# Optimization experiments

Measured on AMD Instinct MI355X. Metric: run time of the kernel, lower is better.

The kernel has to match this reference:

```python
import jax, jax.numpy as jnp
import numpy as np


def setup_inputs() -> dict:
    key = jax.random.key(0)
    k1, k2, k3, k4 = jax.random.split(key, 4)
    B, T, S, D = 256, 16, 32, 768
    return {
        "video_global": jax.random.normal(k1, (B, D), dtype=jnp.float32),
        "text_global": jax.random.normal(k2, (B, D), dtype=jnp.float32),
        "video_local": jax.random.normal(k3, (B, T, D), dtype=jnp.float32),
        "text_local": jax.random.normal(k4, (B, S, D), dtype=jnp.float32),
        "temp": jnp.zeros((1,), dtype=jnp.float32),  # log(1.0)
    }


def reference(video_global, text_global, video_local, text_local, temp):
    B = video_global.shape[0]
    logit_scale = jnp.exp(temp)[0]

    # ---- global contrastive loss ----
    global_sim = logit_scale * (video_global @ text_global.T)  # [B, B]
    diag = jnp.arange(B)
    loss_v2t = -jax.nn.log_softmax(global_sim, axis=1)[diag, diag].mean()
    loss_t2v = -jax.nn.log_softmax(global_sim, axis=0)[diag, diag].mean()
    loss_global = 0.5 * (loss_v2t + loss_t2v)

    # ---- local positive scores ----
    # paired (diagonal) local similarity: [B, T, S]
    sim_pos = logit_scale * jnp.einsum("btd,bsd->bts", video_local, text_local)
    time_weights = jax.nn.softmax(sim_pos.max(axis=-1), axis=-1)  # [B, T]
    pos_scores = (sim_pos.mean(axis=-1) * time_weights).sum(axis=1)  # [B]

    # ---- local negative scores (batched pairwise contraction) ----
    # [B, B, T, S]: video i vs text j, replacing the B*(B-1) tiny einsum loop
    sim_all = logit_scale * jnp.einsum("btd,csd->bcts", video_local, text_local)
    neg_full = (time_weights[:, None, :] * sim_all.mean(axis=-1)).sum(axis=-1)  # [B, B]

    # drop diagonal (i == j), preserving row-major loop order
    rows, cols = np.nonzero(~np.eye(B, dtype=bool))
    neg_scores = neg_full[rows, cols].reshape(B, B - 1)

    logits = jnp.concatenate([pos_scores[:, None], neg_scores], axis=-1)  # [B, B]
    loss_local = -jax.nn.log_softmax(logits, axis=-1)[:, 0].mean()

    return 0.6 * loss_global + 0.4 * loss_local
```

## Files before the change

### kernel.cpp

```cpp
#include <hip/hip_runtime.h>
#include <cmath>

#define BB 256
#define TT 16
#define SS 32
#define DD 768
#define LROW 260

__device__ __forceinline__ void wave_lse(
    const float* __restrict__ cparts, float* __restrict__ out,
    int cm, int row, float w)
{
    const int lane = threadIdx.x & 63;
    float4 x = make_float4(0.f, 0.f, 0.f, 0.f);
    const float* base = cparts + (size_t)cm * 65536 + (size_t)row * 256 + (lane << 2);
#pragma unroll
    for (int p = 0; p < 8; ++p) {
        float4 v = *(const float4*)(base + (size_t)p * 3 * 65536);
        x.x += v.x; x.y += v.y; x.z += v.z; x.w += v.w;
    }
    float m = fmaxf(fmaxf(x.x, x.y), fmaxf(x.z, x.w));
#pragma unroll
    for (int off = 32; off > 0; off >>= 1)
        m = fmaxf(m, __shfl_xor(m, off, 64));
    float e = expf(x.x - m) + expf(x.y - m) + expf(x.z - m) + expf(x.w - m);
#pragma unroll
    for (int off = 32; off > 0; off >>= 1)
        e += __shfl_xor(e, off, 64);
    if (lane == (row >> 2)) {
        float lse = m + logf(e);
        float xd = (row & 2) ? ((row & 1) ? x.w : x.z)
                             : ((row & 1) ? x.y : x.x);
        atomicAdd(out, w * (lse - xd));
    }
}

__global__ __launch_bounds__(512, 4) void hl_k1(
    const float* __restrict__ vl, const float* __restrict__ tl,
    const float* __restrict__ vgp, const float* __restrict__ tgp,
    const float* __restrict__ temp,
    float* __restrict__ vw_ws, float* __restrict__ tb_ws,
    float* __restrict__ cparts, float* __restrict__ out, int out_n)
{
    __shared__ float lds[13024];
    const int tid = threadIdx.x;
    const float lsc = expf(temp[0]);

    if (blockIdx.x < BB) {
        float* smem  = lds;
        float* simb  = lds + 12480;
        float* rmaxb = lds + 12992;
        float* twb   = lds + 13008;
        const int i = blockIdx.x;
        if (i == 0) {
            for (int o = tid; o < out_n; o += 512) out[o] = 0.f;
        }

        const int slice = tid & 15;
        const int g     = tid >> 4;
        const int tgr   = g >> 3;
        const int sg    = g & 7;

        const float* vli = vl + (size_t)i * TT * DD;
        const float* tli = tl + (size_t)i * SS * DD;

        float acc[4][4];
#pragma unroll
        for (int a = 0; a < 4; ++a)
#pragma unroll
            for (int b = 0; b < 4; ++b) acc[a][b] = 0.f;

        float4 pre[6];
#pragma unroll
        for (int k = 0; k < 2; ++k) {
            int f4 = tid + (k << 9);
            pre[k] = *(const float4*)&vli[(f4 >> 6) * DD + ((f4 & 63) << 2)];
        }
#pragma unroll
        for (int k = 0; k < 4; ++k) {
            int f4 = tid + (k << 9);
            pre[2 + k] = *(const float4*)&tli[(f4 >> 6) * DD + ((f4 & 63) << 2)];
        }

        for (int c = 0; c < 3; ++c) {
            __syncthreads();
#pragma unroll
            for (int k = 0; k < 2; ++k) {
                int f4 = tid + (k << 9);
                *(float4*)&smem[(f4 >> 6) * LROW + ((f4 & 63) << 2)] = pre[k];
            }
#pragma unroll
            for (int k = 0; k < 4; ++k) {
                int f4 = tid + (k << 9);
                *(float4*)&smem[(16 + (f4 >> 6)) * LROW + ((f4 & 63) << 2)] = pre[2 + k];
            }
            __syncthreads();
            if (c < 2) {
                const int d0n = (c + 1) << 8;
#pragma unroll
                for (int k = 0; k < 2; ++k) {
                    int f4 = tid + (k << 9);
                    pre[k] = *(const float4*)&vli[(f4 >> 6) * DD + d0n + ((f4 & 63) << 2)];
                }
#pragma unroll
                for (int k = 0; k < 4; ++k) {
                    int f4 = tid + (k << 9);
                    pre[2 + k] = *(const float4*)&tli[(f4 >> 6) * DD + d0n + ((f4 & 63) << 2)];
                }
            }
#pragma unroll
            for (int step = 0; step < 4; ++step) {
                const int db = (slice << 4) + (step << 2);
                float4 av[4], bv[4];
#pragma unroll
                for (int ti = 0; ti < 4; ++ti)
                    av[ti] = *(const float4*)&smem[(tgr * 4 + ti) * LROW + db];
#pragma unroll
                for (int sj = 0; sj < 4; ++sj)
                    bv[sj] = *(const float4*)&smem[(16 + sg * 4 + sj) * LROW + db];
#pragma unroll
                for (int ti = 0; ti < 4; ++ti)
#pragma unroll
                    for (int sj = 0; sj < 4; ++sj)
                        acc[ti][sj] += av[ti].x * bv[sj].x + av[ti].y * bv[sj].y
                                     + av[ti].z * bv[sj].z + av[ti].w * bv[sj].w;
            }
        }
        __syncthreads();

#pragma unroll
        for (int ti = 0; ti < 4; ++ti)
#pragma unroll
            for (int sj = 0; sj < 4; ++sj) {
                int t = tgr * 4 + ti, s = sg * 4 + sj;
                smem[(t * 32 + s) * 17 + slice] = acc[ti][sj];
            }
        __syncthreads();
        {
            float ssum = 0.f;
#pragma unroll
            for (int k = 0; k < 16; ++k) ssum += smem[tid * 17 + k];
            simb[tid] = lsc * ssum;
        }
        __syncthreads();
        if (tid < 16) {
            float m = -3.0e38f;
            for (int s = 0; s < 32; ++s)
                m = fmaxf(m, simb[tid * 32 + ((s + tid) & 31)]);
            rmaxb[tid] = m;
        }
        __syncthreads();
        if (tid == 0) {
            float M = -3.0e38f;
            for (int t = 0; t < 16; ++t) M = fmaxf(M, rmaxb[t]);
            float ssum = 0.f;
            for (int t = 0; t < 16; ++t) {
                float e = expf(rmaxb[t] - M);
                twb[t] = e;
                ssum += e;
            }
            float inv = 1.0f / ssum;
            for (int t = 0; t < 16; ++t) twb[t] *= inv;
        }
        __syncthreads();

        for (int d = tid; d < DD; d += 512) {
            float vwv = 0.f;
#pragma unroll
            for (int t = 0; t < 16; ++t) vwv += twb[t] * vli[t * DD + d];
            vw_ws[(size_t)i * DD + d] = vwv;
            float tbv = 0.f;
#pragma unroll
            for (int s = 0; s < 32; ++s) tbv += tli[s * DD + d];
            tb_ws[(size_t)i * DD + d] = tbv * (1.0f / 32.0f);
        }
    } else {
        float (*As)[68] = (float (*)[68])lds;
        float (*Bs)[68] = (float (*)[68])(lds + 1088);
        float (*Tb)[68] = (float (*)[68])(lds + 2176);
        const int b  = blockIdx.x - BB;
        const int p  = b & 7;
        const int tj = (b >> 3) & 3;
        const int ti = b >> 5;
        const int i0 = ti * 64, j0 = tj * 64, kb0 = p * 96;
        const bool act = tid < 256;
        const int srow = tid >> 2, skq = tid & 3;
        const int tr = tid >> 4, tc = tid & 15;

        float acc[4][4];
#pragma unroll
        for (int r = 0; r < 4; ++r)
#pragma unroll
            for (int cc = 0; cc < 4; ++cc) acc[r][cc] = 0.f;

        float4 a4 = make_float4(0.f, 0.f, 0.f, 0.f), b4 = a4;
        float4 a4n = a4, b4n = b4;
        if (act) {
            a4 = *(const float4*)&vgp[(size_t)(i0 + srow) * DD + kb0 + skq * 4];
            b4 = *(const float4*)&tgp[(size_t)(j0 + srow) * DD + kb0 + skq * 4];
        }
        for (int ch = 0; ch < 6; ++ch) {
            __syncthreads();
            if (act) {
                As[skq * 4 + 0][srow] = a4.x; As[skq * 4 + 1][srow] = a4.y;
                As[skq * 4 + 2][srow] = a4.z; As[skq * 4 + 3][srow] = a4.w;
                Bs[skq * 4 + 0][srow] = b4.x; Bs[skq * 4 + 1][srow] = b4.y;
                Bs[skq * 4 + 2][srow] = b4.z; Bs[skq * 4 + 3][srow] = b4.w;
            }
            __syncthreads();
            if (act && ch < 5) {
                const int kb = kb0 + (ch + 1) * 16;
                a4n = *(const float4*)&vgp[(size_t)(i0 + srow) * DD + kb + skq * 4];
                b4n = *(const float4*)&tgp[(size_t)(j0 + srow) * DD + kb + skq * 4];
            }
            if (act) {
#pragma unroll
                for (int k = 0; k < 16; ++k) {
                    float4 av = *(const float4*)&As[k][tr * 4];
                    float4 bv = *(const float4*)&Bs[k][tc * 4];
                    float ar[4] = {av.x, av.y, av.z, av.w};
                    float br[4] = {bv.x, bv.y, bv.z, bv.w};
#pragma unroll
                    for (int r = 0; r < 4; ++r)
#pragma unroll
                        for (int cc = 0; cc < 4; ++cc)
                            acc[r][cc] += ar[r] * br[cc];
                }
            }
            a4 = a4n; b4 = b4n;
        }

        if (act) {
            float* Cp = cparts + ((size_t)p * 3 + 1) * 65536;
#pragma unroll
            for (int r = 0; r < 4; ++r) {
                float4 v = {acc[r][0] * lsc, acc[r][1] * lsc,
                            acc[r][2] * lsc, acc[r][3] * lsc};
                *(float4*)&Cp[(size_t)(i0 + tr * 4 + r) * 256 + j0 + tc * 4] = v;
            }
        }
        __syncthreads();
        if (act) {
#pragma unroll
            for (int r = 0; r < 4; ++r)
#pragma unroll
                for (int cc = 0; cc < 4; ++cc)
                    Tb[tc * 4 + cc][tr * 4 + r] = acc[r][cc] * lsc;
        }
        __syncthreads();
        if (act) {
            float* Ct = cparts + ((size_t)p * 3 + 2) * 65536;
#pragma unroll
            for (int r = 0; r < 4; ++r) {
                float4 v = *(const float4*)&Tb[tr * 4 + r][tc * 4];
                *(float4*)&Ct[(size_t)(j0 + tr * 4 + r) * 256 + i0 + tc * 4] = v;
            }
        }
    }
}

__global__ __launch_bounds__(256) void hl_k2(
    const float* __restrict__ vw, const float* __restrict__ tbm,
    const float* __restrict__ temp, float* __restrict__ cparts,
    float* __restrict__ out)
{
    const int tid = threadIdx.x;
    const int b   = blockIdx.x;
    if (b < 128) {
        __shared__ float As[16][68];
        __shared__ float Bs[16][68];
        const float lsc = expf(temp[0]);
        const int p = b & 7, tj = (b >> 3) & 3, ti = b >> 5;
        const int i0 = ti * 64, j0 = tj * 64, kb0 = p * 96;
        const int srow = tid >> 2, skq = tid & 3;
        const int tr = tid >> 4, tc = tid & 15;

        float acc[4][4];
#pragma unroll
        for (int r = 0; r < 4; ++r)
#pragma unroll
            for (int cc = 0; cc < 4; ++cc) acc[r][cc] = 0.f;

        float4 a4 = *(const float4*)&vw [(size_t)(i0 + srow) * DD + kb0 + skq * 4];
        float4 b4 = *(const float4*)&tbm[(size_t)(j0 + srow) * DD + kb0 + skq * 4];
        float4 a4n = a4, b4n = b4;
        for (int ch = 0; ch < 6; ++ch) {
            __syncthreads();
            As[skq * 4 + 0][srow] = a4.x; As[skq * 4 + 1][srow] = a4.y;
            As[skq * 4 + 2][srow] = a4.z; As[skq * 4 + 3][srow] = a4.w;
            Bs[skq * 4 + 0][srow] = b4.x; Bs[skq * 4 + 1][srow] = b4.y;
            Bs[skq * 4 + 2][srow] = b4.z; Bs[skq * 4 + 3][srow] = b4.w;
            __syncthreads();
            if (ch < 5) {
                const int kb = kb0 + (ch + 1) * 16;
                a4n = *(const float4*)&vw [(size_t)(i0 + srow) * DD + kb + skq * 4];
                b4n = *(const float4*)&tbm[(size_t)(j0 + srow) * DD + kb + skq * 4];
            }
#pragma unroll
            for (int k = 0; k < 16; ++k) {
                float4 av = *(const float4*)&As[k][tr * 4];
                float4 bv = *(const float4*)&Bs[k][tc * 4];
                float ar[4] = {av.x, av.y, av.z, av.w};
                float br[4] = {bv.x, bv.y, bv.z, bv.w};
#pragma unroll
                for (int r = 0; r < 4; ++r)
#pragma unroll
                    for (int cc = 0; cc < 4; ++cc)
                        acc[r][cc] += ar[r] * br[cc];
            }
            a4 = a4n; b4 = b4n;
        }

        float* Cp = cparts + (size_t)p * 3 * 65536;
#pragma unroll
        for (int r = 0; r < 4; ++r) {
            float4 v = {acc[r][0] * lsc, acc[r][1] * lsc,
                        acc[r][2] * lsc, acc[r][3] * lsc};
            *(float4*)&Cp[(size_t)(i0 + tr * 4 + r) * 256 + j0 + tc * 4] = v;
        }
    } else {
        const int idx = b - 128;
        const int cm  = 1 + (idx >> 6);
        const int row = ((idx & 63) << 2) + (tid >> 6);
        wave_lse(cparts, out, cm, row, 0.3f / 256.0f);
    }
}

__global__ __launch_bounds__(256) void hl_k3(
    const float* __restrict__ cparts, float* __restrict__ out)
{
    const int row = (blockIdx.x << 2) + (threadIdx.x >> 6);
    wave_lse(cparts, out, 0, row, 0.4f / 256.0f);
}

extern "C" void kernel_launch(void* const* d_in, const int* in_sizes, int n_in,
                              void* d_out, int out_size, void* d_ws, size_t ws_size,
                              hipStream_t stream)
{
    const float* vg   = (const float*)d_in[0];
    const float* tg   = (const float*)d_in[1];
    const float* vl   = (const float*)d_in[2];
    const float* tl   = (const float*)d_in[3];
    const float* temp = (const float*)d_in[4];
    float* out = (float*)d_out;

    float* vw     = (float*)d_ws;
    float* tbw    = vw + (size_t)BB * DD;
    float* cparts = tbw + (size_t)BB * DD;

    hl_k1<<<dim3(BB + 128), dim3(512), 0, stream>>>(vl, tl, vg, tg, temp,
                                                    vw, tbw, cparts, out, out_size);
    hl_k2<<<dim3(256), dim3(256), 0, stream>>>(vw, tbw, temp, cparts, out);
    hl_k3<<<dim3(64),  dim3(256), 0, stream>>>(cparts, out);
}
```

Measured before the change: 123.2 us.

## Pack two GEMM tiles per 512-thread block and drop register prefetch in local sim

The global-GEMM blocks in the first kernel previously left half their 512 threads idle; now each block runs two 64x64 tile jobs, one per 256-thread half, each with its own shared-memory region, which halves the extra block count. The second kernel likewise uses 512-thread blocks holding two GEMM jobs or eight LSE rows, and the third kernel handles eight rows per block. The local-similarity loop drops register-staged prefetch of the next chunk in favour of direct global-to-LDS copies, and the occupancy hint in launch_bounds is removed. This trades latency hiding for lower register pressure, and the larger per-block shared memory may reduce how many blocks fit per CU.

```diff
diff --git a/kernel.cpp b/kernel.cpp
--- a/kernel.cpp
+++ b/kernel.cpp
@@ -35,14 +35,14 @@
     }
 }
 
-__global__ __launch_bounds__(512, 4) void hl_k1(
+__global__ __launch_bounds__(512) void hl_k1(
     const float* __restrict__ vl, const float* __restrict__ tl,
     const float* __restrict__ vgp, const float* __restrict__ tgp,
     const float* __restrict__ temp,
     float* __restrict__ vw_ws, float* __restrict__ tb_ws,
     float* __restrict__ cparts, float* __restrict__ out, int out_n)
 {
-    __shared__ float lds[13024];
+    __shared__ float lds[13056];
     const int tid = threadIdx.x;
     const float lsc = expf(temp[0]);
 
@@ -70,44 +70,23 @@
 #pragma unroll
             for (int b = 0; b < 4; ++b) acc[a][b] = 0.f;
 
-        float4 pre[6];
-#pragma unroll
-        for (int k = 0; k < 2; ++k) {
-            int f4 = tid + (k << 9);
-            pre[k] = *(const float4*)&vli[(f4 >> 6) * DD + ((f4 & 63) << 2)];
-        }
-#pragma unroll
-        for (int k = 0; k < 4; ++k) {
-            int f4 = tid + (k << 9);
-            pre[2 + k] = *(const float4*)&tli[(f4 >> 6) * DD + ((f4 & 63) << 2)];
-        }
-
         for (int c = 0; c < 3; ++c) {
-            __syncthreads();
+            const int d0 = c << 8;
 #pragma unroll
             for (int k = 0; k < 2; ++k) {
                 int f4 = tid + (k << 9);
-                *(float4*)&smem[(f4 >> 6) * LROW + ((f4 & 63) << 2)] = pre[k];
+                int r  = f4 >> 6;
+                int dc = (f4 & 63) << 2;
+                *(float4*)&smem[r * LROW + dc] = *(const float4*)&vli[r * DD + d0 + dc];
             }
 #pragma unroll
             for (int k = 0; k < 4; ++k) {
                 int f4 = tid + (k << 9);
-                *(float4*)&smem[(16 + (f4 >> 6)) * LROW + ((f4 & 63) << 2)] = pre[2 + k];
-            }
-            __syncthreads();
-            if (c < 2) {
-                const int d0n = (c + 1) << 8;
-#pragma unroll
-                for (int k = 0; k < 2; ++k) {
-                    int f4 = tid + (k << 9);
-                    pre[k] = *(const float4*)&vli[(f4 >> 6) * DD + d0n + ((f4 & 63) << 2)];
-                }
-#pragma unroll
-                for (int k = 0; k < 4; ++k) {
-                    int f4 = tid + (k << 9);
-                    pre[2 + k] = *(const float4*)&tli[(f4 >> 6) * DD + d0n + ((f4 & 63) << 2)];
-                }
-            }
+                int r  = f4 >> 6;
+                int dc = (f4 & 63) << 2;
+                *(float4*)&smem[(16 + r) * LROW + dc] = *(const float4*)&tli[r * DD + d0 + dc];
+            }
+            __syncthreads();
 #pragma unroll
             for (int step = 0; step < 4; ++step) {
                 const int db = (slice << 4) + (step << 2);
@@ -125,8 +104,8 @@
                         acc[ti][sj] += av[ti].x * bv[sj].x + av[ti].y * bv[sj].y
                                      + av[ti].z * bv[sj].z + av[ti].w * bv[sj].w;
             }
-        }
-        __syncthreads();
+            __syncthreads();
+        }
 
 #pragma unroll
         for (int ti = 0; ti < 4; ++ti)
@@ -175,17 +154,20 @@
             tb_ws[(size_t)i * DD + d] = tbv * (1.0f / 32.0f);
         }
     } else {
-        float (*As)[68] = (float (*)[68])lds;
-        float (*Bs)[68] = (float (*)[68])(lds + 1088);
-        float (*Tb)[68] = (float (*)[68])(lds + 2176);
-        const int b  = blockIdx.x - BB;
-        const int p  = b & 7;
-        const int tj = (b >> 3) & 3;
-        const int ti = b >> 5;
+        const int h   = tid >> 8;
+        const int t   = tid & 255;
+        const int job = ((blockIdx.x - BB) << 1) | h;
+        float* base = lds + h * 6528;
+        float (*As)[68] = (float (*)[68])base;
+        float (*Bs)[68] = (float (*)[68])(base + 1088);
+        float (*Tb)[68] = (float (*)[68])(base + 2176);
+
+        const int p  = job & 7;
+        const int tj = (job >> 3) & 3;
+        const int ti = job >> 5;
         const int i0 = ti * 64, j0 = tj * 64, kb0 = p * 96;
-        const bool act = tid < 256;
-        const int srow = tid >> 2, skq = tid & 3;
-        const int tr = tid >> 4, tc = tid & 15;
+        const int srow = t >> 2, skq = t & 3;
+        const int tr = t >> 4, tc = t & 15;
 
         float acc[4][4];
 #pragma unroll
@@ -193,96 +175,8 @@
 #pragma unroll
             for (int cc = 0; cc < 4; ++cc) acc[r][cc] = 0.f;
 
-        float4 a4 = make_float4(0.f, 0.f, 0.f, 0.f), b4 = a4;
-        float4 a4n = a4, b4n = b4;
-        if (act) {
-            a4 = *(const float4*)&vgp[(size_t)(i0 + srow) * DD + kb0 + skq * 4];
-            b4 = *(const float4*)&tgp[(size_t)(j0 + srow) * DD + kb0 + skq * 4];
-        }
-        for (int ch = 0; ch < 6; ++ch) {
-            __syncthreads();
-            if (act) {
-                As[skq * 4 + 0][srow] = a4.x; As[skq * 4 + 1][srow] = a4.y;
-                As[skq * 4 + 2][srow] = a4.z; As[skq * 4 + 3][srow] = a4.w;
-                Bs[skq * 4 + 0][srow] = b4.x; Bs[skq * 4 + 1][srow] = b4.y;
-                Bs[skq * 4 + 2][srow] = b4.z; Bs[skq * 4 + 3][srow] = b4.w;
-            }
-            __syncthreads();
-            if (act && ch < 5) {
-                const int kb = kb0 + (ch + 1) * 16;
-                a4n = *(const float4*)&vgp[(size_t)(i0 + srow) * DD + kb + skq * 4];
-                b4n = *(const float4*)&tgp[(size_t)(j0 + srow) * DD + kb + skq * 4];
-            }
-            if (act) {
-#pragma unroll
-                for (int k = 0; k < 16; ++k) {
-                    float4 av = *(const float4*)&As[k][tr * 4];
-                    float4 bv = *(const float4*)&Bs[k][tc * 4];
-                    float ar[4] = {av.x, av.y, av.z, av.w};
-                    float br[4] = {bv.x, bv.y, bv.z, bv.w};
-#pragma unroll
-                    for (int r = 0; r < 4; ++r)
-#pragma unroll
-                        for (int cc = 0; cc < 4; ++cc)
-                            acc[r][cc] += ar[r] * br[cc];
-                }
-            }
-            a4 = a4n; b4 = b4n;
-        }
-
-        if (act) {
-            float* Cp = cparts + ((size_t)p * 3 + 1) * 65536;
-#pragma unroll
-            for (int r = 0; r < 4; ++r) {
-                float4 v = {acc[r][0] * lsc, acc[r][1] * lsc,
-                            acc[r][2] * lsc, acc[r][3] * lsc};
-                *(float4*)&Cp[(size_t)(i0 + tr * 4 + r) * 256 + j0 + tc * 4] = v;
-            }
-        }
-        __syncthreads();
-        if (act) {
-#pragma unroll
-            for (int r = 0; r < 4; ++r)
-#pragma unroll
-                for (int cc = 0; cc < 4; ++cc)
-                    Tb[tc * 4 + cc][tr * 4 + r] = acc[r][cc] * lsc;
-        }
-        __syncthreads();
-        if (act) {
-            float* Ct = cparts + ((size_t)p * 3 + 2) * 65536;
-#pragma unroll
-            for (int r = 0; r < 4; ++r) {
-                float4 v = *(const float4*)&Tb[tr * 4 + r][tc * 4];
-                *(float4*)&Ct[(size_t)(j0 + tr * 4 + r) * 256 + i0 + tc * 4] = v;
-            }
-        }
-    }
-}
-
-__global__ __launch_bounds__(256) void hl_k2(
-    const float* __restrict__ vw, const float* __restrict__ tbm,
-    const float* __restrict__ temp, float* __restrict__ cparts,
-    float* __restrict__ out)
-{
-    const int tid = threadIdx.x;
-    const int b   = blockIdx.x;
-    if (b < 128) {
-        __shared__ float As[16][68];
-        __shared__ float Bs[16][68];
-        const float lsc = expf(temp[0]);
-        const int p = b & 7, tj = (b >> 3) & 3, ti = b >> 5;
-        const int i0 = ti * 64, j0 = tj * 64, kb0 = p * 96;
-        const int srow = tid >> 2, skq = tid & 3;
-        const int tr = tid >> 4, tc = tid & 15;
-
-        float acc[4][4];
-#pragma unroll
-        for (int r = 0; r < 4; ++r)
-#pragma unroll
-            for (int cc = 0; cc < 4; ++cc) acc[r][cc] = 0.f;
-
-        float4 a4 = *(const float4*)&vw [(size_t)(i0 + srow) * DD + kb0 + skq * 4];
-        float4 b4 = *(const float4*)&tbm[(size_t)(j0 + srow) * DD + kb0 + skq * 4];
+        float4 a4 = *(const float4*)&vgp[(size_t)(i0 + srow) * DD + kb0 + skq * 4];
+        float4 b4 = *(const float4*)&tgp[(size_t)(j0 + srow) * DD + kb0 + skq * 4];
         float4 a4n = a4, b4n = b4;
         for (int ch = 0; ch < 6; ++ch) {
             __syncthreads();
@@ -293,8 +187,8 @@
             __syncthreads();
             if (ch < 5) {
                 const int kb = kb0 + (ch + 1) * 16;
-                a4n = *(const float4*)&vw [(size_t)(i0 + srow) * DD + kb + skq * 4];
-                b4n = *(const float4*)&tbm[(size_t)(j0 + srow) * DD + kb + skq * 4];
+                a4n = *(const float4*)&vgp[(size_t)(i0 + srow) * DD + kb + skq * 4];
+                b4n = *(const float4*)&tgp[(size_t)(j0 + srow) * DD + kb + skq * 4];
             }
 #pragma unroll
             for (int k = 0; k < 16; ++k) {
@@ -311,25 +205,107 @@
             a4 = a4n; b4 = b4n;
         }
 
-        float* Cp = cparts + (size_t)p * 3 * 65536;
+        float* Cp = cparts + ((size_t)p * 3 + 1) * 65536;
 #pragma unroll
         for (int r = 0; r < 4; ++r) {
             float4 v = {acc[r][0] * lsc, acc[r][1] * lsc,
                         acc[r][2] * lsc, acc[r][3] * lsc};
             *(float4*)&Cp[(size_t)(i0 + tr * 4 + r) * 256 + j0 + tc * 4] = v;
         }
+        __syncthreads();
+#pragma unroll
+        for (int r = 0; r < 4; ++r)
+#pragma unroll
+            for (int cc = 0; cc < 4; ++cc)
+                Tb[tc * 4 + cc][tr * 4 + r] = acc[r][cc] * lsc;
+        __syncthreads();
+        float* Ct = cparts + ((size_t)p * 3 + 2) * 65536;
+#pragma unroll
+        for (int r = 0; r < 4; ++r) {
+            float4 v = *(const float4*)&Tb[tr * 4 + r][tc * 4];
+            *(float4*)&Ct[(size_t)(j0 + tr * 4 + r) * 256 + i0 + tc * 4] = v;
+        }
+    }
+}
+
+__global__ __launch_bounds__(512) void hl_k2(
+    const float* __restrict__ vw, const float* __restrict__ tbm,
+    const float* __restrict__ temp, float* __restrict__ cparts,
+    float* __restrict__ out)
+{
+    __shared__ float lds2[4352];
+    const int tid = threadIdx.x;
+    if (blockIdx.x < 64) {
+        const float lsc = expf(temp[0]);
+        const int h   = tid >> 8;
+        const int t   = tid & 255;
+        const int job = (blockIdx.x << 1) | h;
+        float* base = lds2 + h * 2176;
+        float (*As)[68] = (float (*)[68])base;
+        float (*Bs)[68] = (float (*)[68])(base + 1088);
+
+        const int p  = job & 7;
+        const int tj = (job >> 3) & 3;
+        const int ti = job >> 5;
+        const int i0 = ti * 64, j0 = tj * 64, kb0 = p * 96;
+        const int srow = t >> 2, skq = t & 3;
+        const int tr = t >> 4, tc = t & 15;
+
+        float acc[4][4];
+#pragma unroll
+        for (int r = 0; r < 4; ++r)
+#pragma unroll
+            for (int cc = 0; cc < 4; ++cc) acc[r][cc] = 0.f;
+
+        float4 a4 = *(const float4*)&vw [(size_t)(i0 + srow) * DD + kb0 + skq * 4];
+        float4 b4 = *(const float4*)&tbm[(size_t)(j0 + srow) * DD + kb0 + skq * 4];
+        float4 a4n = a4, b4n = b4;
+        for (int ch = 0; ch < 6; ++ch) {
+            __syncthreads();
+            As[skq * 4 + 0][srow] = a4.x; As[skq * 4 + 1][srow] = a4.y;
+            As[skq * 4 + 2][srow] = a4.z; As[skq * 4 + 3][srow] = a4.w;
+            Bs[skq * 4 + 0][srow] = b4.x; Bs[skq * 4 + 1][srow] = b4.y;
+            Bs[skq * 4 + 2][srow] = b4.z; Bs[skq * 4 + 3][srow] = b4.w;
+            __syncthreads();
+            if (ch < 5) {
+                const int kb = kb0 + (ch + 1) * 16;
+                a4n = *(const float4*)&vw [(size_t)(i0 + srow) * DD + kb + skq * 4];
+                b4n = *(const float4*)&tbm[(size_t)(j0 + srow) * DD + kb + skq * 4];
+            }
+#pragma unroll
+            for (int k = 0; k < 16; ++k) {
+                float4 av = *(const float4*)&As[k][tr * 4];
+                float4 bv = *(const float4*)&Bs[k][tc * 4];
+                float ar[4] = {av.x, av.y, av.z, av.w};
+                float br[4] = {bv.x, bv.y, bv.z, bv.w};
+#pragma unroll
+                for (int r = 0; r < 4; ++r)
+#pragma unroll
+                    for (int cc = 0; cc < 4; ++cc)
+                        acc[r][cc] += ar[r] * br[cc];
+            }
+            a4 = a4n; b4 = b4n;
+        }
+
+        float* Cp = cparts + (size_t)p * 3 * 65536;
+#pragma unroll
+        for (int r = 0; r < 4; ++r) {
+            float4 v = {acc[r][0] * lsc, acc[r][1] * lsc,
+                        acc[r][2] * lsc, acc[r][3] * lsc};
+            *(float4*)&Cp[(size_t)(i0 + tr * 4 + r) * 256 + j0 + tc * 4] = v;
+        }
     } else {
-        const int idx = b - 128;
-        const int cm  = 1 + (idx >> 6);
-        const int row = ((idx & 63) << 2) + (tid >> 6);
+        const int rr  = ((blockIdx.x - 64) << 3) + (tid >> 6);
+        const int cm  = 1 + (rr >> 8);
+        const int row = rr & 255;
         wave_lse(cparts, out, cm, row, 0.3f / 256.0f);
     }
 }
 
-__global__ __launch_bounds__(256) void hl_k3(
+__global__ __launch_bounds__(512) void hl_k3(
     const float* __restrict__ cparts, float* __restrict__ out)
 {
-    const int row = (blockIdx.x << 2) + (threadIdx.x >> 6);
+    const int row = (blockIdx.x << 3) + (threadIdx.x >> 6);
     wave_lse(cparts, out, 0, row, 0.4f / 256.0f);
 }
 
@@ -348,8 +324,8 @@
     float* tbw    = vw + (size_t)BB * DD;
     float* cparts = tbw + (size_t)BB * DD;
 
-    hl_k1<<<dim3(BB + 128), dim3(512), 0, stream>>>(vl, tl, vg, tg, temp,
-                                                    vw, tbw, cparts, out, out_size);
-    hl_k2<<<dim3(256), dim3(256), 0, stream>>>(vw, tbw, temp, cparts, out);
-    hl_k3<<<dim3(64),  dim3(256), 0, stream>>>(cparts, out);
-}
+    hl_k1<<<dim3(BB + 64), dim3(512), 0, stream>>>(vl, tl, vg, tg, temp,
+                                                   vw, tbw, cparts, out, out_size);
+    hl_k2<<<dim3(128), dim3(512), 0, stream>>>(vw, tbw, temp, cparts, out);
+    hl_k3<<<dim3(32),  dim3(512), 0, stream>>>(cparts, out);
+}
```

Measured after the change: 120.9 us. About the same (-1.8%).
